# Performance work log

Hardware: AMD Instinct MI355X
Metric: run time of the kernel (lower is better)

Reference implementation:

```python
import jax, jax.numpy as jnp
import numpy as np

B, H, T, DH = 2, 16, 2048, 64
SCALE = DH ** -0.5


def setup_inputs() -> dict:
    key = jax.random.key(0)
    kq, kk, kv = jax.random.split(key, 3)
    q = jax.random.normal(kq, (B, H, T, DH), dtype=jnp.float32)
    k = jax.random.normal(kk, (B, H, T, DH), dtype=jnp.float32)
    v = jax.random.normal(kv, (B, H, T, DH), dtype=jnp.float32)
    attention_mask = jnp.ones((B, T), dtype=bool)  # (B, Tk) padding mask, True=keep
    causal_mask = jnp.tril(jnp.ones((T, T), dtype=bool))[None, None]  # (1,1,Tq,Tk)
    return {"q": q, "k": k, "v": v, "attention_mask": attention_mask,
            "causal_mask": causal_mask}


def _attend(q, k, v, attention_mask, causal_mask):
    # scores in fp32 as in the torch module
    scores = jnp.einsum("bhqd,bhkd->bhqk", q.astype(jnp.float32),
                        k.astype(jnp.float32)) * SCALE
    neg_inf = jnp.float32(-jnp.inf)
    # (B,Tk) bool padding mask -> (B,1,1,Tk), broadcasts over Tq
    pad = attention_mask[:, None, None, :]
    scores = jnp.where(pad, scores, neg_inf)
    scores = jnp.where(causal_mask, scores, neg_inf)
    attn = jax.nn.softmax(scores, axis=-1).astype(q.dtype)
    ctx = jnp.einsum("bhqk,bhkd->bhqd", attn, v)  # (B,H,Tq,Dh)
    Bq, Hq, Tq, Dh = ctx.shape
    return ctx.transpose(0, 2, 1, 3).reshape(Bq, Tq, Hq * Dh)


def reference(q, k, v, attention_mask, causal_mask):
    return _attend(q, k, v, attention_mask, causal_mask)
```

## Files before the change

kernel.cpp:

```cpp
#include <hip/hip_runtime.h>


constexpr int Bc = 2, Hc = 16, Tc = 2048, Dc = 64;
constexpr float QSCALE = 0.125f * 1.44269504088896340736f;

typedef __attribute__((__ext_vector_type__(8))) __bf16 bf16x8;
typedef __attribute__((__ext_vector_type__(4))) __bf16 bf16x4;
typedef __attribute__((__ext_vector_type__(4))) float f32x4;

__global__ __launch_bounds__(256, 4) void attn_fwd_kernel(
    const float* __restrict__ Q,
    const float* __restrict__ K,
    const float* __restrict__ V,
    float* __restrict__ O)
{
  const int tid  = threadIdx.x;
  const int wave = tid >> 6;
  const int lane = tid & 63;
  const int l16  = lane & 15;
  const int g    = lane >> 4;

  const int bid  = blockIdx.x;
  const int head = bid & 31;
  const int vv   = bid >> 5;
  const int aq   = vv >> 3;
  const int bq   = vv & 7;
  int qtile;
  switch (aq) {
    case 0:  qtile = bq;      break;
    case 1:  qtile = 15 - bq; break;
    case 2:  qtile = 16 + bq; break;
    default: qtile = 31 - bq; break;
  }

  const int b = head >> 4, h = head & 15;
  const int q0 = qtile * 64 + wave * 16;

  const size_t hoff = (size_t)head * Tc * Dc;
  const float* Qb = Q + hoff;
  const float* Kb = K + hoff;
  const float* Vb = V + hoff;

  __shared__ __bf16 Kl[64 * 64];
  __shared__ __bf16 Vt[64 * 64];

  bf16x8 qf[2];
  {
    const float* qrow = Qb + (size_t)(q0 + l16) * Dc + g * 8;
    #pragma unroll
    for (int c = 0; c < 2; ++c)
      #pragma unroll
      for (int j = 0; j < 8; ++j)
        qf[c][j] = (__bf16)(qrow[c * 32 + j] * QSCALE);
  }

  f32x4 o_acc[4] = {};
  float m_run = -1e30f, l_run = 0.f;

  const int krow = tid >> 2;
  const int seg  = tid & 3;
  const int kswz = (krow & 7) << 4;
  const int vkb  = tid >> 4;
  const int vdb  = tid & 15;

  const int n_iter = qtile + 1;

  float4 kreg[4], vreg[4];
  {
    const float4* kp4 = (const float4*)(Kb + (size_t)krow * Dc + seg * 16);
    #pragma unroll
    for (int c = 0; c < 4; ++c) kreg[c] = kp4[c];
    const float* vb0 = Vb + (size_t)(vkb * 4) * Dc + vdb * 4;
    #pragma unroll
    for (int r = 0; r < 4; ++r) vreg[r] = *(const float4*)(vb0 + r * Dc);
  }

  for (int it = 0; it < n_iter; ++it) {
    __syncthreads();

    #pragma unroll
    for (int hh = 0; hh < 2; ++hh) {
      const float* x0 = (const float*)&kreg[2 * hh];
      const float* x1 = (const float*)&kreg[2 * hh + 1];
      bf16x8 t;
      #pragma unroll
      for (int j = 0; j < 4; ++j) { t[j] = (__bf16)x0[j]; t[4 + j] = (__bf16)x1[j]; }
      *(bf16x8*)((char*)Kl + krow * 128 + ((seg * 32 + hh * 16) ^ kswz)) = t;
    }
    #pragma unroll
    for (int i = 0; i < 4; ++i) {
      bf16x4 t;
      #pragma unroll
      for (int r = 0; r < 4; ++r) t[r] = (__bf16)((const float*)&vreg[r])[i];
      const int d = vdb * 4 + i;
      *(bf16x4*)((char*)Vt + vkb * 512 + ((d * 8) ^ (vkb << 3))) = t;
    }
    __syncthreads();

    if (it + 1 < n_iter) {
      const int kv1 = (it + 1) * 64;
      const float4* kp4 = (const float4*)(Kb + (size_t)(kv1 + krow) * Dc + seg * 16);
      #pragma unroll
      for (int c = 0; c < 4; ++c) kreg[c] = kp4[c];
      const float* vb0 = Vb + (size_t)(kv1 + vkb * 4) * Dc + vdb * 4;
      #pragma unroll
      for (int r = 0; r < 4; ++r) vreg[r] = *(const float4*)(vb0 + r * Dc);
    }

    const bool partial = (it == qtile);
    const int  ns = partial ? (wave + 1) : 4;

    f32x4 sacc[4];
    #pragma unroll
    for (int s = 0; s < 4; ++s) {
      if (s < ns) {
        f32x4 z = {0.f, 0.f, 0.f, 0.f};
        const int row = s * 16 + l16;
        const char* kb = (const char*)Kl + row * 128;
        const int swz = (row & 7) << 4;
        bf16x8 k0 = *(const bf16x8*)(kb + ((g * 16) ^ swz));
        bf16x8 k1 = *(const bf16x8*)(kb + ((64 + g * 16) ^ swz));
        z = __builtin_amdgcn_mfma_f32_16x16x32_bf16(k0, qf[0], z, 0, 0, 0);
        z = __builtin_amdgcn_mfma_f32_16x16x32_bf16(k1, qf[1], z, 0, 0, 0);
        sacc[s] = z;
      } else {
        sacc[s] = f32x4{-INFINITY, -INFINITY, -INFINITY, -INFINITY};
      }
    }
    if (partial) {
      #pragma unroll
      for (int s = 0; s < 4; ++s)
        #pragma unroll
        for (int r = 0; r < 4; ++r)
          if (s * 16 + g * 4 + r > wave * 16 + l16) sacc[s][r] = -INFINITY;
    }

    float mx = -INFINITY;
    #pragma unroll
    for (int s = 0; s < 4; ++s)
      #pragma unroll
      for (int r = 0; r < 4; ++r) mx = fmaxf(mx, sacc[s][r]);
    mx = fmaxf(mx, __shfl_xor(mx, 16, 64));
    mx = fmaxf(mx, __shfl_xor(mx, 32, 64));
    const float mn = fmaxf(m_run, mx);
    const float f  = __builtin_amdgcn_exp2f(m_run - mn);
    m_run = mn;

    float sum = 0.f;
    bf16x8 pa[2];
    #pragma unroll
    for (int c = 0; c < 2; ++c)
      #pragma unroll
      for (int j = 0; j < 8; ++j) {
        const float pv = __builtin_amdgcn_exp2f(sacc[2 * c + (j >> 2)][j & 3] - mn);
        sum += pv;
        pa[c][j] = (__bf16)pv;
      }
    sum += __shfl_xor(sum, 16, 64);
    sum += __shfl_xor(sum, 32, 64);
    l_run = l_run * f + sum;

    #pragma unroll
    for (int r = 0; r < 4; ++r) {
      const float fo = __shfl(f, g * 4 + r, 64);
      #pragma unroll
      for (int dt = 0; dt < 4; ++dt) o_acc[dt][r] *= fo;
    }

    #pragma unroll
    for (int dt = 0; dt < 4; ++dt) {
      const int d = dt * 16 + l16;
      #pragma unroll
      for (int c = 0; c < 2; ++c) {
        const int kc0 = 8 * c + g;
        const int kc1 = 8 * c + 4 + g;
        union { bf16x8 v8; bf16x4 v4[2]; } u;
        u.v4[0] = *(const bf16x4*)((char*)Vt + kc0 * 512 + ((d * 8) ^ (kc0 << 3)));
        u.v4[1] = *(const bf16x4*)((char*)Vt + kc1 * 512 + ((d * 8) ^ (kc1 << 3)));
        o_acc[dt] = __builtin_amdgcn_mfma_f32_16x16x32_bf16(pa[c], u.v8, o_acc[dt], 0, 0, 0);
      }
    }
  }

  #pragma unroll
  for (int r = 0; r < 4; ++r) {
    const float il = __shfl(l_run, g * 4 + r, 64);
    const float inv = 1.f / il;
    float* orow = O + ((size_t)b * Tc + (q0 + g * 4 + r)) * (Hc * Dc) + h * Dc;
    #pragma unroll
    for (int dt = 0; dt < 4; ++dt)
      orow[dt * 16 + l16] = o_acc[dt][r] * inv;
  }
}

extern "C" void kernel_launch(void* const* d_in, const int* in_sizes, int n_in,
                              void* d_out, int out_size, void* d_ws, size_t ws_size,
                              hipStream_t stream) {
  const float* q = (const float*)d_in[0];
  const float* k = (const float*)d_in[1];
  const float* v = (const float*)d_in[2];
  float* out = (float*)d_out;

  dim3 grid(Bc * Hc * (Tc / 64));
  dim3 block(256);
  hipLaunchKernelGGL(attn_fwd_kernel, grid, block, 0, stream, q, k, v, out);
}
```

Measured before the change: 53.27 us.

## Pair causal q-tiles per block, add lazy rescale, V swizzle, MFMA priority

Each block now handles two q-tiles, pr and 31-pr, so every block does equal causal work, and the grid shrinks to 512 blocks. The online softmax skips rescaling o_acc unless the row max grows by more than 8 (log2 units). The V transpose in LDS gets an extra XOR swizzle to reduce bank conflicts, and s_setprio brackets the MFMA sections. Q loads are vectorised to float4. With half as many blocks, occupancy across 256 CUs may drop. The threshold-based rescale lets unnormalised values grow up to 2^8, which stays safe in fp32 and bf16.

```diff
diff --git a/kernel.cpp b/kernel.cpp
--- a/kernel.cpp
+++ b/kernel.cpp
@@ -22,19 +22,8 @@
 
   const int bid  = blockIdx.x;
   const int head = bid & 31;
-  const int vv   = bid >> 5;
-  const int aq   = vv >> 3;
-  const int bq   = vv & 7;
-  int qtile;
-  switch (aq) {
-    case 0:  qtile = bq;      break;
-    case 1:  qtile = 15 - bq; break;
-    case 2:  qtile = 16 + bq; break;
-    default: qtile = 31 - bq; break;
-  }
-
+  const int pr   = bid >> 5;
   const int b = head >> 4, h = head & 15;
-  const int q0 = qtile * 64 + wave * 16;
 
   const size_t hoff = (size_t)head * Tc * Dc;
   const float* Qb = Q + hoff;
@@ -43,153 +32,174 @@
 
   __shared__ __bf16 Kl[64 * 64];
   __shared__ __bf16 Vt[64 * 64];
-
-  bf16x8 qf[2];
-  {
-    const float* qrow = Qb + (size_t)(q0 + l16) * Dc + g * 8;
-    #pragma unroll
-    for (int c = 0; c < 2; ++c)
-      #pragma unroll
-      for (int j = 0; j < 8; ++j)
-        qf[c][j] = (__bf16)(qrow[c * 32 + j] * QSCALE);
-  }
-
-  f32x4 o_acc[4] = {};
-  float m_run = -1e30f, l_run = 0.f;
 
   const int krow = tid >> 2;
   const int seg  = tid & 3;
   const int kswz = (krow & 7) << 4;
   const int vkb  = tid >> 4;
   const int vdb  = tid & 15;
-
-  const int n_iter = qtile + 1;
+  const int vwx  = (vdb >> 2) << 3;
 
   float4 kreg[4], vreg[4];
-  {
-    const float4* kp4 = (const float4*)(Kb + (size_t)krow * Dc + seg * 16);
-    #pragma unroll
-    for (int c = 0; c < 4; ++c) kreg[c] = kp4[c];
-    const float* vb0 = Vb + (size_t)(vkb * 4) * Dc + vdb * 4;
-    #pragma unroll
-    for (int r = 0; r < 4; ++r) vreg[r] = *(const float4*)(vb0 + r * Dc);
-  }
-
-  for (int it = 0; it < n_iter; ++it) {
-    __syncthreads();
-
-    #pragma unroll
-    for (int hh = 0; hh < 2; ++hh) {
-      const float* x0 = (const float*)&kreg[2 * hh];
-      const float* x1 = (const float*)&kreg[2 * hh + 1];
-      bf16x8 t;
-      #pragma unroll
-      for (int j = 0; j < 4; ++j) { t[j] = (__bf16)x0[j]; t[4 + j] = (__bf16)x1[j]; }
-      *(bf16x8*)((char*)Kl + krow * 128 + ((seg * 32 + hh * 16) ^ kswz)) = t;
-    }
-    #pragma unroll
-    for (int i = 0; i < 4; ++i) {
-      bf16x4 t;
-      #pragma unroll
-      for (int r = 0; r < 4; ++r) t[r] = (__bf16)((const float*)&vreg[r])[i];
-      const int d = vdb * 4 + i;
-      *(bf16x4*)((char*)Vt + vkb * 512 + ((d * 8) ^ (vkb << 3))) = t;
-    }
-    __syncthreads();
-
-    if (it + 1 < n_iter) {
-      const int kv1 = (it + 1) * 64;
-      const float4* kp4 = (const float4*)(Kb + (size_t)(kv1 + krow) * Dc + seg * 16);
+
+  for (int ph = 0; ph < 2; ++ph) {
+    const int qtile = ph ? (31 - pr) : pr;
+    const int q0 = qtile * 64 + wave * 16;
+
+    bf16x8 qf[2];
+    {
+      const float4* qp = (const float4*)(Qb + (size_t)(q0 + l16) * Dc + g * 8);
+      #pragma unroll
+      for (int c = 0; c < 2; ++c) {
+        float4 x0 = qp[c * 8], x1 = qp[c * 8 + 1];
+        const float* f0 = (const float*)&x0;
+        const float* f1 = (const float*)&x1;
+        #pragma unroll
+        for (int j = 0; j < 4; ++j) {
+          qf[c][j]     = (__bf16)(f0[j] * QSCALE);
+          qf[c][4 + j] = (__bf16)(f1[j] * QSCALE);
+        }
+      }
+    }
+
+    f32x4 o_acc[4] = {};
+    float m_run = -1e30f, l_run = 0.f;
+
+    const int n_iter = qtile + 1;
+
+    {
+      const float4* kp4 = (const float4*)(Kb + (size_t)krow * Dc + seg * 16);
       #pragma unroll
       for (int c = 0; c < 4; ++c) kreg[c] = kp4[c];
-      const float* vb0 = Vb + (size_t)(kv1 + vkb * 4) * Dc + vdb * 4;
+      const float* vb0 = Vb + (size_t)(vkb * 4) * Dc + vdb * 4;
       #pragma unroll
       for (int r = 0; r < 4; ++r) vreg[r] = *(const float4*)(vb0 + r * Dc);
     }
 
-    const bool partial = (it == qtile);
-    const int  ns = partial ? (wave + 1) : 4;
-
-    f32x4 sacc[4];
-    #pragma unroll
-    for (int s = 0; s < 4; ++s) {
-      if (s < ns) {
-        f32x4 z = {0.f, 0.f, 0.f, 0.f};
-        const int row = s * 16 + l16;
-        const char* kb = (const char*)Kl + row * 128;
-        const int swz = (row & 7) << 4;
-        bf16x8 k0 = *(const bf16x8*)(kb + ((g * 16) ^ swz));
-        bf16x8 k1 = *(const bf16x8*)(kb + ((64 + g * 16) ^ swz));
-        z = __builtin_amdgcn_mfma_f32_16x16x32_bf16(k0, qf[0], z, 0, 0, 0);
-        z = __builtin_amdgcn_mfma_f32_16x16x32_bf16(k1, qf[1], z, 0, 0, 0);
-        sacc[s] = z;
-      } else {
-        sacc[s] = f32x4{-INFINITY, -INFINITY, -INFINITY, -INFINITY};
-      }
-    }
-    if (partial) {
+    for (int it = 0; it < n_iter; ++it) {
+      __syncthreads();
+
+      #pragma unroll
+      for (int hh = 0; hh < 2; ++hh) {
+        const float* x0 = (const float*)&kreg[2 * hh];
+        const float* x1 = (const float*)&kreg[2 * hh + 1];
+        bf16x8 t;
+        #pragma unroll
+        for (int j = 0; j < 4; ++j) { t[j] = (__bf16)x0[j]; t[4 + j] = (__bf16)x1[j]; }
+        *(bf16x8*)((char*)Kl + krow * 128 + ((seg * 32 + hh * 16) ^ kswz)) = t;
+      }
+      #pragma unroll
+      for (int i = 0; i < 4; ++i) {
+        bf16x4 t;
+        #pragma unroll
+        for (int r = 0; r < 4; ++r) t[r] = (__bf16)((const float*)&vreg[r])[i];
+        const int d = vdb * 4 + i;
+        *(bf16x4*)((char*)Vt + vkb * 512 + ((d * 8) ^ (vkb << 3) ^ vwx)) = t;
+      }
+      __syncthreads();
+
+      if (it + 1 < n_iter) {
+        const int kv1 = (it + 1) * 64;
+        const float4* kp4 = (const float4*)(Kb + (size_t)(kv1 + krow) * Dc + seg * 16);
+        #pragma unroll
+        for (int c = 0; c < 4; ++c) kreg[c] = kp4[c];
+        const float* vb0 = Vb + (size_t)(kv1 + vkb * 4) * Dc + vdb * 4;
+        #pragma unroll
+        for (int r = 0; r < 4; ++r) vreg[r] = *(const float4*)(vb0 + r * Dc);
+      }
+
+      const bool partial = (it == qtile);
+      const int  ns = partial ? (wave + 1) : 4;
+
+      f32x4 sacc[4];
+      __builtin_amdgcn_s_setprio(1);
+      #pragma unroll
+      for (int s = 0; s < 4; ++s) {
+        if (s < ns) {
+          f32x4 z = {0.f, 0.f, 0.f, 0.f};
+          const int row = s * 16 + l16;
+          const char* kb = (const char*)Kl + row * 128;
+          const int swz = (row & 7) << 4;
+          bf16x8 k0 = *(const bf16x8*)(kb + ((g * 16) ^ swz));
+          bf16x8 k1 = *(const bf16x8*)(kb + ((64 + g * 16) ^ swz));
+          z = __builtin_amdgcn_mfma_f32_16x16x32_bf16(k0, qf[0], z, 0, 0, 0);
+          z = __builtin_amdgcn_mfma_f32_16x16x32_bf16(k1, qf[1], z, 0, 0, 0);
+          sacc[s] = z;
+        } else {
+          sacc[s] = f32x4{-INFINITY, -INFINITY, -INFINITY, -INFINITY};
+        }
+      }
+      __builtin_amdgcn_s_setprio(0);
+      if (partial) {
+        #pragma unroll
+        for (int s = 0; s < 4; ++s)
+          #pragma unroll
+          for (int r = 0; r < 4; ++r)
+            if (s * 16 + g * 4 + r > wave * 16 + l16) sacc[s][r] = -INFINITY;
+      }
+
+      float mx = -INFINITY;
       #pragma unroll
       for (int s = 0; s < 4; ++s)
         #pragma unroll
-        for (int r = 0; r < 4; ++r)
-          if (s * 16 + g * 4 + r > wave * 16 + l16) sacc[s][r] = -INFINITY;
-    }
-
-    float mx = -INFINITY;
-    #pragma unroll
-    for (int s = 0; s < 4; ++s)
-      #pragma unroll
-      for (int r = 0; r < 4; ++r) mx = fmaxf(mx, sacc[s][r]);
-    mx = fmaxf(mx, __shfl_xor(mx, 16, 64));
-    mx = fmaxf(mx, __shfl_xor(mx, 32, 64));
-    const float mn = fmaxf(m_run, mx);
-    const float f  = __builtin_amdgcn_exp2f(m_run - mn);
-    m_run = mn;
-
-    float sum = 0.f;
-    bf16x8 pa[2];
-    #pragma unroll
-    for (int c = 0; c < 2; ++c)
-      #pragma unroll
-      for (int j = 0; j < 8; ++j) {
-        const float pv = __builtin_amdgcn_exp2f(sacc[2 * c + (j >> 2)][j & 3] - mn);
-        sum += pv;
-        pa[c][j] = (__bf16)pv;
-      }
-    sum += __shfl_xor(sum, 16, 64);
-    sum += __shfl_xor(sum, 32, 64);
-    l_run = l_run * f + sum;
+        for (int r = 0; r < 4; ++r) mx = fmaxf(mx, sacc[s][r]);
+      mx = fmaxf(mx, __shfl_xor(mx, 16, 64));
+      mx = fmaxf(mx, __shfl_xor(mx, 32, 64));
+
+      if (!__all(mx <= m_run + 8.0f)) {
+        const float mn = fmaxf(m_run, mx);
+        const float f  = __builtin_amdgcn_exp2f(m_run - mn);
+        m_run = mn;
+        l_run *= f;
+        #pragma unroll
+        for (int r = 0; r < 4; ++r) {
+          const float fo = __shfl(f, g * 4 + r, 64);
+          #pragma unroll
+          for (int dt = 0; dt < 4; ++dt) o_acc[dt][r] *= fo;
+        }
+      }
+
+      float sum = 0.f;
+      bf16x8 pa[2];
+      #pragma unroll
+      for (int c = 0; c < 2; ++c)
+        #pragma unroll
+        for (int j = 0; j < 8; ++j) {
+          const float pv = __builtin_amdgcn_exp2f(sacc[2 * c + (j >> 2)][j & 3] - m_run);
+          sum += pv;
+          pa[c][j] = (__bf16)pv;
+        }
+      sum += __shfl_xor(sum, 16, 64);
+      sum += __shfl_xor(sum, 32, 64);
+      l_run += sum;
+
+      __builtin_amdgcn_s_setprio(1);
+      #pragma unroll
+      for (int dt = 0; dt < 4; ++dt) {
+        const int d = dt * 16 + l16;
+        const int dx = (dt & 3) << 3;
+        #pragma unroll
+        for (int c = 0; c < 2; ++c) {
+          const int kc0 = 8 * c + g;
+          const int kc1 = 8 * c + 4 + g;
+          union { bf16x8 v8; bf16x4 v4[2]; } u;
+          u.v4[0] = *(const bf16x4*)((char*)Vt + kc0 * 512 + ((d * 8) ^ (kc0 << 3) ^ dx));
+          u.v4[1] = *(const bf16x4*)((char*)Vt + kc1 * 512 + ((d * 8) ^ (kc1 << 3) ^ dx));
+          o_acc[dt] = __builtin_amdgcn_mfma_f32_16x16x32_bf16(pa[c], u.v8, o_acc[dt], 0, 0, 0);
+        }
+      }
+      __builtin_amdgcn_s_setprio(0);
+    }
 
     #pragma unroll
     for (int r = 0; r < 4; ++r) {
-      const float fo = __shfl(f, g * 4 + r, 64);
-      #pragma unroll
-      for (int dt = 0; dt < 4; ++dt) o_acc[dt][r] *= fo;
-    }
-
-    #pragma unroll
-    for (int dt = 0; dt < 4; ++dt) {
-      const int d = dt * 16 + l16;
-      #pragma unroll
-      for (int c = 0; c < 2; ++c) {
-        const int kc0 = 8 * c + g;
-        const int kc1 = 8 * c + 4 + g;
-        union { bf16x8 v8; bf16x4 v4[2]; } u;
-        u.v4[0] = *(const bf16x4*)((char*)Vt + kc0 * 512 + ((d * 8) ^ (kc0 << 3)));
-        u.v4[1] = *(const bf16x4*)((char*)Vt + kc1 * 512 + ((d * 8) ^ (kc1 << 3)));
-        o_acc[dt] = __builtin_amdgcn_mfma_f32_16x16x32_bf16(pa[c], u.v8, o_acc[dt], 0, 0, 0);
-      }
-    }
-  }
-
-  #pragma unroll
-  for (int r = 0; r < 4; ++r) {
-    const float il = __shfl(l_run, g * 4 + r, 64);
-    const float inv = 1.f / il;
-    float* orow = O + ((size_t)b * Tc + (q0 + g * 4 + r)) * (Hc * Dc) + h * Dc;
-    #pragma unroll
-    for (int dt = 0; dt < 4; ++dt)
-      orow[dt * 16 + l16] = o_acc[dt][r] * inv;
+      const float il = __shfl(l_run, g * 4 + r, 64);
+      const float inv = 1.f / il;
+      float* orow = O + ((size_t)b * Tc + (q0 + g * 4 + r)) * (Hc * Dc) + h * Dc;
+      #pragma unroll
+      for (int dt = 0; dt < 4; ++dt)
+        orow[dt * 16 + l16] = o_acc[dt][r] * inv;
+    }
   }
 }
 
@@ -201,7 +211,7 @@
   const float* v = (const float*)d_in[2];
   float* out = (float*)d_out;
 
-  dim3 grid(Bc * Hc * (Tc / 64));
+  dim3 grid(512);
   dim3 block(256);
   hipLaunchKernelGGL(attn_fwd_kernel, grid, block, 0, stream, q, k, v, out);
 }
```

After: 53.09 us. Within noise of the previous version (-0.3%).
